# Kernel tuning notes

Measured on AMD Instinct MI355X. Metric: run time of the kernel, lower is better.

## Reference

```python
import jax, jax.numpy as jnp
from jax import lax
import numpy as np

NBC, NAC, KF, RHO = 14, 45, 52, 0.05
KT = np.arange(0.8, 0, -1.0 / 64, dtype=np.float32)[None, :]  # (1, 52) AC kernel time axis
K = KT.shape[1]


def _sigm(x, off, slope):
    return jax.nn.sigmoid(slope * (x - off))


def _ac_kernel(log_tr, log_td, kt):
    tr = jnp.exp(log_tr)[:, None]  # (nAC,1)
    td = jnp.exp(log_td)[:, None]
    k = jnp.exp(-kt / td) - jnp.exp(-(td + tr) / (td * tr) * kt)  # (nAC,K)
    return k / jnp.linalg.norm(k, axis=1, keepdims=True)


def setup_inputs() -> dict:
    key = jax.random.key(0)
    ks = jax.random.split(key, 12)
    B, T = 64, 4096
    n = 0.01  # noise_init_scale
    return {
        "x": jax.random.normal(ks[0], (B, T), jnp.float32) * 0.5,
        "bc_kernels": jax.random.normal(ks[1], (NBC, KF), jnp.float32) * 0.1,
        "log_sigmoid_slope": jnp.log(2.0) + n * jax.random.normal(ks[2], (NBC,), jnp.float32),
        "sigmoid_offset": 1.5 + n * jax.random.normal(ks[3], (NBC,), jnp.float32),
        "log_bc_ac_weight": jnp.log(1.0 / NBC) + n * jax.random.normal(ks[4], (NAC, NBC), jnp.float32),
        "log_ac_tau_rise": jnp.log(0.1) + n * jax.random.normal(ks[5], (NAC,), jnp.float32),
        "log_ac_tau_decay": jnp.log(0.1) + n * jax.random.normal(ks[6], (NAC,), jnp.float32),
        "log_ac_sigmoid_slope": jnp.log(2.0) + n * jax.random.normal(ks[7], (NAC,), jnp.float32),
        "ac_sigmoid_offset": 1.5 + n * jax.random.normal(ks[8], (NAC,), jnp.float32),
        "log_ac_bc_weight": jnp.log(0.01) + n * jax.random.normal(ks[9], (NBC, NAC), jnp.float32),
        "out_scale": jnp.ones((NBC,), jnp.float32),
    }


def reference(x, bc_kernels, log_sigmoid_slope, sigmoid_offset, log_bc_ac_weight,
              log_ac_tau_rise, log_ac_tau_decay, log_ac_sigmoid_slope,
              ac_sigmoid_offset, log_ac_bc_weight, out_scale):
    B, T = x.shape
    kt = jnp.asarray(KT)
    # linear_filter: causal conv of stimulus with per-BC kernels -> (T, B, nBC)
    xf = lax.conv_general_dilated(x[:, None, :], bc_kernels[:, None, :], (1,), [(KF - 1, 0)])
    xf = jnp.transpose(xf, (2, 0, 1))  # (T, B, nBC)

    slope = jnp.exp(log_sigmoid_slope)
    ac_slope = jnp.exp(log_ac_sigmoid_slope)
    bc_ac_w = jnp.exp(log_bc_ac_weight)          # (nAC, nBC)
    ac_bc_w = -jnp.exp(log_ac_bc_weight)         # (nBC, nAC)
    ack = _ac_kernel(log_ac_tau_rise, log_ac_tau_decay, kt)  # (nAC, K)

    # --- plain LNR branch (no feedback) ---
    prob_lnr = _sigm(xf, sigmoid_offset, slope)

    def lnr_step(pool, p):
        pool2 = pool + (1.0 - pool) * RHO
        rel = p * pool2
        return pool2 - rel, rel

    _, rel_lnr = lax.scan(lnr_step, jnp.ones((B, NBC), x.dtype), prob_lnr)
    y_lnr = (out_scale * rel_lnr).transpose(1, 0, 2)  # (B, T, nBC)

    # --- BCN branch with AC feedback recurrence ---
    def bcn_step(carry, xt):
        pool, prev_rel, buf = carry
        # append previous release (track_release[i-1]) to sliding window (oldest first)
        buf = jnp.concatenate([buf[..., 1:], prev_rel[..., None]], axis=-1)  # (B, nBC, K)
        drive = jnp.einsum('ak,ab,nbk->na', ack, bc_ac_w, buf)               # (B, nAC)
        ac_out = _sigm(drive, ac_sigmoid_offset, ac_slope)
        fb = ac_out @ ac_bc_w.T                                              # (B, nBC)
        prob = _sigm(xt + fb, sigmoid_offset, slope)
        pool2 = pool + (1.0 - pool) * RHO
        rel = prob * pool2
        return (pool2 - rel, rel, buf), (rel, fb, ac_out)

    init = (jnp.ones((B, NBC), x.dtype), jnp.zeros((B, NBC), x.dtype), jnp.zeros((B, NBC, K), x.dtype))
    _, (rel, fb, ac_out) = lax.scan(bcn_step, init, xf)
    y_bcn = (out_scale * rel).transpose(1, 0, 2)  # (B, T, nBC)
    return y_bcn, fb.transpose(1, 0, 2), ac_out.transpose(1, 0, 2), y_lnr
```

## Files before the change

kernel.cpp:

```cpp
#include <hip/hip_runtime.h>
#include <hip/hip_fp16.h>

#define NBC 14
#define NAC 45
#define KF  52
#define RHO 0.05f
#define TT  4096
#define BB  64
#define CHC 64
#define WU  44
#define NPAIR 32
#define NTW (WU + CHC)
#define SPAN (WU + 2*CHC)
#define XPAD 176
#define RING 52
#define LOG2E 1.44269504f

typedef __fp16 v2h __attribute__((ext_vector_type(2)));
typedef float  f2  __attribute__((ext_vector_type(2)));
typedef int    i2v __attribute__((ext_vector_type(2)));

__device__ __forceinline__ v2h bch(unsigned u) { return __builtin_bit_cast(v2h, u); }
__device__ __forceinline__ unsigned bcu(v2h h) { return __builtin_bit_cast(unsigned, h); }
__device__ __forceinline__ v2h pk2(float lo, float hi) {
#if __has_builtin(__builtin_amdgcn_cvt_pkrtz)
  return __builtin_bit_cast(v2h, __builtin_amdgcn_cvt_pkrtz(lo, hi));
#else
  v2h r; r[0] = (__fp16)lo; r[1] = (__fp16)hi; return r;
#endif
}
__device__ __forceinline__ v2h xsum16h(v2h v) {
#if __has_builtin(__builtin_amdgcn_permlane16_swap)
  i2v r = __builtin_amdgcn_permlane16_swap((int)bcu(v), (int)bcu(v), false, false);
  return bch((unsigned)r[0]) + bch((unsigned)r[1]);
#else
  return v + bch((unsigned)__builtin_amdgcn_ds_swizzle((int)bcu(v), (16 << 10) | 0x1f));
#endif
}
__device__ __forceinline__ v2h xsum32h(v2h v) {
#if __has_builtin(__builtin_amdgcn_permlane32_swap)
  i2v r = __builtin_amdgcn_permlane32_swap((int)bcu(v), (int)bcu(v), false, false);
  return bch((unsigned)r[0]) + bch((unsigned)r[1]);
#else
  return v + bch((unsigned)__shfl_xor((int)bcu(v), 32));
#endif
}
__device__ __forceinline__ float exp2_f(float x) {
#if __has_builtin(__builtin_amdgcn_exp2f)
  return __builtin_amdgcn_exp2f(x);
#else
  return exp2f(x);
#endif
}

#define POOL_BYTES 14608

__global__ __launch_bounds__(64)
void bcn_kernel(const float* __restrict__ x,
                const float* __restrict__ bck,
                const float* __restrict__ lss,
                const float* __restrict__ soff,
                const float* __restrict__ lbaw,
                const float* __restrict__ ltr,
                const float* __restrict__ ltd,
                const float* __restrict__ lass,
                const float* __restrict__ asoff,
                const float* __restrict__ labw,
                const float* __restrict__ oscale,
                float* __restrict__ out)
{
  __shared__ __align__(16) char pool[POOL_BYTES];
  unsigned* u_ring = (unsigned*)pool;
  float*    x_lds  = (float*)pool;
  __half*   xf_lds = (__half*)(pool + 9360);
  unsigned* acr    = (unsigned*)(pool + 14288);
  unsigned* relr   = (unsigned*)(pool + 14544);

  const int lid   = threadIdx.x;
  const int c16   = lid & 15;
  const int q     = lid >> 4;
  const int blk   = blockIdx.x;
  const int b     = blk >> 5;
  const int p     = blk & 31;
  const int t0A   = p * (2 * CHC);
  const int t_begin = t0A - WU;

  for (int i = lid; i < SPAN + KF - 1; i += 64) {
    int gt = t_begin - (KF - 1) + i;
    x_lds[i] = (gt >= 0) ? x[b * TT + gt] : 0.f;
  }
  __syncthreads();

  for (int ib = 0; ib < 3; ++ib) {
    int tau = lid + (ib << 6);
    if (tau < SPAN) {
      float acc[NBC];
#pragma unroll
      for (int c = 0; c < NBC; ++c) acc[c] = 0.f;
#pragma unroll 4
      for (int k = 0; k < KF; ++k) {
        float xv = x_lds[tau + k];
#pragma unroll
        for (int c = 0; c < NBC; ++c) acc[c] = fmaf(bck[c * KF + k], xv, acc[c]);
      }
#pragma unroll
      for (int c = 0; c < NBC; ++c) xf_lds[c * XPAD + tau] = __float2half(acc[c]);
    }
  }
  __syncthreads();

  for (int i = lid; i < NAC * RING; i += 64) u_ring[i] = 0u;
  if (lid < 64) acr[lid] = 0u;
  if (lid < 16) relr[lid] = 0u;

  float slope2 = 0.f, soff2 = 0.f, osc_c = 0.f;
  f2 poolA; poolA.x = 1.f; poolA.y = 1.f;
  f2 poolB; poolB.x = 1.f; poolB.y = 1.f;
  f2 SA; SA.x = 0.f; SA.y = 0.f;
  f2 SB; SB.x = 0.f; SB.y = 0.f;
  f2 rv2, cn2, co2; rv2.x = rv2.y = cn2.x = cn2.y = co2.x = co2.y = 0.f;
  float Adrv2 = 0.f, Boff2 = 0.f;
  v2h wfbh[16];
  v2h wuh[NBC];
  f2 yst[4], fst[4], lst[4];
  unsigned acst[4];

#pragma unroll
  for (int j = 0; j < 16; ++j) wfbh[j] = pk2(0.f, 0.f);
#pragma unroll
  for (int c = 0; c < NBC; ++c) wuh[c] = pk2(0.f, 0.f);

  if (c16 < NBC) {
    float sl = expf(lss[c16]);
    slope2 = sl * LOG2E;
    soff2  = soff[c16] * sl * LOG2E;
    osc_c  = oscale[c16];
#pragma unroll
    for (int j = 0; j < 16; ++j) {
      int a = 16 * q + j;
      if (a < NAC) { float w = -expf(labw[c16 * NAC + a]); wfbh[j] = pk2(w, w); }
    }
  }
  if (lid < NAC) {
    float tr = expf(ltr[lid]);
    float td = expf(ltd[lid]);
    float a1 = 1.f / td;
    float gg = (td + tr) / (td * tr);
    rv2.x = expf(-a1 * 0.015625f);  rv2.y = expf(-gg * 0.015625f);
    cn2.x = expf(-a1 * 0.003125f);  cn2.y = expf(-gg * 0.003125f);
    co2.x = expf(-a1 * 0.815625f);  co2.y = expf(-gg * 0.815625f);
    float nrm = 0.f;
    for (int k = 0; k < KF; ++k) {
      float kt = 0.8f - (float)k * 0.015625f;
      float d = expf(-a1 * kt) - expf(-gg * kt);
      nrm = fmaf(d, d, nrm);
    }
    float inorm  = 1.f / sqrtf(nrm);
    float aslope = expf(lass[lid]);
    Adrv2 = aslope * inorm * LOG2E;
    Boff2 = aslope * asoff[lid] * LOG2E;
#pragma unroll
    for (int c = 0; c < NBC; ++c) {
      float w = expf(lbaw[lid * NBC + c]);
      wuh[c] = pk2(w, w);
    }
  }

  float* yb  = out;
  float* fbp = out + (size_t)BB * TT * NBC;
  float* acp = out + 2 * (size_t)BB * TT * NBC;
  float* ylp = out + 2 * (size_t)BB * TT * NBC + (size_t)BB * TT * NAC;

  __syncthreads();

  auto step = [&](int slot4, int rslot, float xfA, float xfB, float uoA, float uoB,
                  bool emit) __attribute__((always_inline)) {
    float mzA = fmaf(-Adrv2, SA.x - SA.y, Boff2);
    float mzB = fmaf(-Adrv2, SB.x - SB.y, Boff2);
    float acA = __fdividef(1.f, 1.f + exp2_f(mzA));
    float acB = __fdividef(1.f, 1.f + exp2_f(mzB));
    if (lid < NAC) acr[lid] = bcu(pk2(acA, acB));

    const uint4* ab = (const uint4*)(acr + (q << 4));
    uint4 A0 = ab[0], A1 = ab[1], A2 = ab[2], A3 = ab[3];
    v2h g0 = wfbh[0] * bch(A0.x);
    v2h g1 = wfbh[1] * bch(A0.y);
    g0 += wfbh[2]  * bch(A0.z);  g1 += wfbh[3]  * bch(A0.w);
    g0 += wfbh[4]  * bch(A1.x);  g1 += wfbh[5]  * bch(A1.y);
    g0 += wfbh[6]  * bch(A1.z);  g1 += wfbh[7]  * bch(A1.w);
    g0 += wfbh[8]  * bch(A2.x);  g1 += wfbh[9]  * bch(A2.y);
    g0 += wfbh[10] * bch(A2.z);  g1 += wfbh[11] * bch(A2.w);
    g0 += wfbh[12] * bch(A3.x);  g1 += wfbh[13] * bch(A3.y);
    g0 += wfbh[14] * bch(A3.z);  g1 += wfbh[15] * bch(A3.w);
    v2h gs = xsum32h(xsum16h(g0 + g1));
    float fbA = (float)gs[0], fbB = (float)gs[1];

    float mlzA = fmaf(-slope2, xfA, soff2);
    float mpzA = fmaf(-slope2, fbA, mlzA);
    float mlzB = fmaf(-slope2, xfB, soff2);
    float mpzB = fmaf(-slope2, fbB, mlzB);
    f2 pvA, pvB;
    pvA.x = __fdividef(1.f, 1.f + exp2_f(mpzA));
    pvA.y = __fdividef(1.f, 1.f + exp2_f(mlzA));
    pvB.x = __fdividef(1.f, 1.f + exp2_f(mpzB));
    pvB.y = __fdividef(1.f, 1.f + exp2_f(mlzB));
    f2 p2A = poolA * (1.f - RHO) + RHO;
    f2 p2B = poolB * (1.f - RHO) + RHO;
    f2 rvA = pvA * p2A, rvB = pvB * p2B;
    poolA = p2A - rvA;  poolB = p2B - rvB;
    if (lid < NBC) relr[lid] = bcu(pk2(rvA.x, rvB.x));
    if (emit) {
      f2 t1; t1.x = osc_c * rvA.x; t1.y = osc_c * rvB.x; yst[slot4] = t1;
      f2 t2; t2.x = fbA;           t2.y = fbB;           fst[slot4] = t2;
      f2 t3; t3.x = osc_c * rvA.y; t3.y = osc_c * rvB.y; lst[slot4] = t3;
      acst[slot4] = bcu(pk2(acA, acB));
    }

    const uint4* rb = (const uint4*)relr;
    uint4 R0 = rb[0], R1 = rb[1], R2 = rb[2], R3 = rb[3];
    v2h h0 = wuh[0] * bch(R0.x);
    v2h h1 = wuh[1] * bch(R0.y);
    h0 += wuh[2]  * bch(R0.z);  h1 += wuh[3]  * bch(R0.w);
    h0 += wuh[4]  * bch(R1.x);  h1 += wuh[5]  * bch(R1.y);
    h0 += wuh[6]  * bch(R1.z);  h1 += wuh[7]  * bch(R1.w);
    h0 += wuh[8]  * bch(R2.x);  h1 += wuh[9]  * bch(R2.y);
    h0 += wuh[10] * bch(R2.z);  h1 += wuh[11] * bch(R2.w);
    h0 += wuh[12] * bch(R3.x);  h1 += wuh[13] * bch(R3.y);
    v2h uh = h0 + h1;
    float uA = (float)uh[0], uB = (float)uh[1];
    if (lid < NAC) {
      u_ring[lid * RING + rslot] = bcu(uh);
      SA = SA * rv2 + (cn2 * uA - co2 * uoA);
      SB = SB * rv2 + (cn2 * uB - co2 * uoB);
    }
  };

  auto group = [&](int s4, int r4, bool emit) __attribute__((always_inline)) {
    uint2 xa = *(const uint2*)&xf_lds[c16 * XPAD + s4];
    uint2 xb = *(const uint2*)&xf_lds[c16 * XPAD + s4 + CHC];
    int roff = ((lid < NAC) ? lid : 0) * RING + r4;
    uint4 ur = *(const uint4*)&u_ring[roff];
    v2h xA01 = bch(xa.x), xA23 = bch(xa.y);
    v2h xB01 = bch(xb.x), xB23 = bch(xb.y);
    v2h u0 = bch(ur.x), u1 = bch(ur.y), u2 = bch(ur.z), u3 = bch(ur.w);
    step(0, r4 + 0, (float)xA01[0], (float)xB01[0], (float)u0[0], (float)u0[1], emit);
    step(1, r4 + 1, (float)xA01[1], (float)xB01[1], (float)u1[0], (float)u1[1], emit);
    step(2, r4 + 2, (float)xA23[0], (float)xB23[0], (float)u2[0], (float)u2[1], emit);
    step(3, r4 + 3, (float)xA23[1], (float)xB23[1], (float)u3[0], (float)u3[1], emit);
  };

  int r4 = 0;
  for (int s4 = 0; s4 < WU; s4 += 4) {
    group(s4, r4, false);
    r4 += 4; if (r4 == RING) r4 = 0;
  }

  if (p == 0) {
    SA.x = 0.f; SA.y = 0.f;
    poolA.x = 1.f; poolA.y = 1.f;
    for (int i = lid; i < NAC * RING; i += 64) u_ring[i] &= 0xFFFF0000u;
  }

  for (int s4 = WU; s4 < NTW; s4 += 4) {
    group(s4, r4, true);
    r4 += 4; if (r4 == RING) r4 = 0;

    int tgA = t0A + (s4 - WU);
    size_t baseA = (size_t)b * TT + tgA;
    size_t obA = baseA * NBC + c16;
    size_t oaA = baseA * NAC + lid;
    if (lid < NBC) {
#pragma unroll
      for (int sl = 0; sl < 4; ++sl) {
        yb [obA + sl * NBC]                     = yst[sl].x;
        yb [obA + (size_t)CHC * NBC + sl * NBC] = yst[sl].y;
        fbp[obA + sl * NBC]                     = fst[sl].x;
        fbp[obA + (size_t)CHC * NBC + sl * NBC] = fst[sl].y;
        ylp[obA + sl * NBC]                     = lst[sl].x;
        ylp[obA + (size_t)CHC * NBC + sl * NBC] = lst[sl].y;
      }
    }
    if (lid < NAC) {
#pragma unroll
      for (int sl = 0; sl < 4; ++sl) {
        v2h h = bch(acst[sl]);
        acp[oaA + sl * NAC]                     = (float)h[0];
        acp[oaA + (size_t)CHC * NAC + sl * NAC] = (float)h[1];
      }
    }
  }
}

extern "C" void kernel_launch(void* const* d_in, const int* in_sizes, int n_in,
                              void* d_out, int out_size, void* d_ws, size_t ws_size,
                              hipStream_t stream) {
  (void)in_sizes; (void)n_in; (void)d_ws; (void)ws_size; (void)out_size;
  bcn_kernel<<<dim3(BB * NPAIR), dim3(64), 0, stream>>>(
      (const float*)d_in[0],
      (const float*)d_in[1],
      (const float*)d_in[2],
      (const float*)d_in[3],
      (const float*)d_in[4],
      (const float*)d_in[5],
      (const float*)d_in[6],
      (const float*)d_in[7],
      (const float*)d_in[8],
      (const float*)d_in[9],
      (const float*)d_in[10],
      (float*)d_out);
}
```

Baseline: 107.8 us.

## Split BCN and LNR sigmoid paths across lane rows; pad AC ring stride

Instead of having every lane evaluate both the feedback (BCN) and no-feedback (LNR) release sigmoids for both chunks, lanes in even 16-lane rows now compute the BCN path and lanes in odd rows compute the LNR path, selected by a row mask on the feedback term. This halves the per-step exp/reciprocal work and the per-lane pool state, and the LNR outputs are written by lanes 16..29. The AC ring buffer row stride is padded from 52 to 54 words and its quad read split into two 8-byte reads, meant to reduce LDS bank conflicts at the cost of slightly more LDS. It also changes the p==0 reset to only touch the A-half of the pool.

```diff
diff --git a/kernel.cpp b/kernel.cpp
--- a/kernel.cpp
+++ b/kernel.cpp
@@ -14,6 +14,7 @@
 #define SPAN (WU + 2*CHC)
 #define XPAD 176
 #define RING 52
+#define RINGP 54
 #define LOG2E 1.44269504f
 
 typedef __fp16 v2h __attribute__((ext_vector_type(2)));
@@ -53,7 +54,7 @@
 #endif
 }
 
-#define POOL_BYTES 14608
+#define POOL_BYTES 14976
 
 __global__ __launch_bounds__(64)
 void bcn_kernel(const float* __restrict__ x,
@@ -72,13 +73,14 @@
   __shared__ __align__(16) char pool[POOL_BYTES];
   unsigned* u_ring = (unsigned*)pool;
   float*    x_lds  = (float*)pool;
-  __half*   xf_lds = (__half*)(pool + 9360);
-  unsigned* acr    = (unsigned*)(pool + 14288);
-  unsigned* relr   = (unsigned*)(pool + 14544);
+  __half*   xf_lds = (__half*)(pool + 9720);
+  unsigned* acr    = (unsigned*)(pool + 14656);
+  unsigned* relr   = (unsigned*)(pool + 14912);
 
   const int lid   = threadIdx.x;
   const int c16   = lid & 15;
   const int q     = lid >> 4;
+  const float rowm = (q & 1) ? 0.f : 1.f;
   const int blk   = blockIdx.x;
   const int b     = blk >> 5;
   const int p     = blk & 31;
@@ -109,20 +111,19 @@
   }
   __syncthreads();
 
-  for (int i = lid; i < NAC * RING; i += 64) u_ring[i] = 0u;
+  for (int i = lid; i < NAC * RINGP; i += 64) u_ring[i] = 0u;
   if (lid < 64) acr[lid] = 0u;
   if (lid < 16) relr[lid] = 0u;
 
   float slope2 = 0.f, soff2 = 0.f, osc_c = 0.f;
-  f2 poolA; poolA.x = 1.f; poolA.y = 1.f;
-  f2 poolB; poolB.x = 1.f; poolB.y = 1.f;
+  f2 poolP; poolP.x = 1.f; poolP.y = 1.f;
   f2 SA; SA.x = 0.f; SA.y = 0.f;
   f2 SB; SB.x = 0.f; SB.y = 0.f;
   f2 rv2, cn2, co2; rv2.x = rv2.y = cn2.x = cn2.y = co2.x = co2.y = 0.f;
   float Adrv2 = 0.f, Boff2 = 0.f;
   v2h wfbh[16];
   v2h wuh[NBC];
-  f2 yst[4], fst[4], lst[4];
+  f2 yst[4], fst[4];
   unsigned acst[4];
 
 #pragma unroll
@@ -195,24 +196,18 @@
     v2h gs = xsum32h(xsum16h(g0 + g1));
     float fbA = (float)gs[0], fbB = (float)gs[1];
 
-    float mlzA = fmaf(-slope2, xfA, soff2);
-    float mpzA = fmaf(-slope2, fbA, mlzA);
-    float mlzB = fmaf(-slope2, xfB, soff2);
-    float mpzB = fmaf(-slope2, fbB, mlzB);
-    f2 pvA, pvB;
-    pvA.x = __fdividef(1.f, 1.f + exp2_f(mpzA));
-    pvA.y = __fdividef(1.f, 1.f + exp2_f(mlzA));
-    pvB.x = __fdividef(1.f, 1.f + exp2_f(mpzB));
-    pvB.y = __fdividef(1.f, 1.f + exp2_f(mlzB));
-    f2 p2A = poolA * (1.f - RHO) + RHO;
-    f2 p2B = poolB * (1.f - RHO) + RHO;
-    f2 rvA = pvA * p2A, rvB = pvB * p2B;
-    poolA = p2A - rvA;  poolB = p2B - rvB;
-    if (lid < NBC) relr[lid] = bcu(pk2(rvA.x, rvB.x));
+    float mA = fmaf(-slope2, fmaf(rowm, fbA, xfA), soff2);
+    float mB = fmaf(-slope2, fmaf(rowm, fbB, xfB), soff2);
+    f2 pv;
+    pv.x = __fdividef(1.f, 1.f + exp2_f(mA));
+    pv.y = __fdividef(1.f, 1.f + exp2_f(mB));
+    f2 p2 = poolP * (1.f - RHO) + RHO;
+    f2 relP = pv * p2;
+    poolP = p2 - relP;
+    if (lid < NBC) relr[lid] = bcu(pk2(relP.x, relP.y));
     if (emit) {
-      f2 t1; t1.x = osc_c * rvA.x; t1.y = osc_c * rvB.x; yst[slot4] = t1;
-      f2 t2; t2.x = fbA;           t2.y = fbB;           fst[slot4] = t2;
-      f2 t3; t3.x = osc_c * rvA.y; t3.y = osc_c * rvB.y; lst[slot4] = t3;
+      yst[slot4] = relP * osc_c;
+      f2 t; t.x = fbA; t.y = fbB; fst[slot4] = t;
       acst[slot4] = bcu(pk2(acA, acB));
     }
 
@@ -229,7 +224,7 @@
     v2h uh = h0 + h1;
     float uA = (float)uh[0], uB = (float)uh[1];
     if (lid < NAC) {
-      u_ring[lid * RING + rslot] = bcu(uh);
+      u_ring[lid * RINGP + rslot] = bcu(uh);
       SA = SA * rv2 + (cn2 * uA - co2 * uoA);
       SB = SB * rv2 + (cn2 * uB - co2 * uoB);
     }
@@ -238,11 +233,12 @@
   auto group = [&](int s4, int r4, bool emit) __attribute__((always_inline)) {
     uint2 xa = *(const uint2*)&xf_lds[c16 * XPAD + s4];
     uint2 xb = *(const uint2*)&xf_lds[c16 * XPAD + s4 + CHC];
-    int roff = ((lid < NAC) ? lid : 0) * RING + r4;
-    uint4 ur = *(const uint4*)&u_ring[roff];
+    int roff = ((lid < NAC) ? lid : 0) * RINGP + r4;
+    uint2 ur01 = *(const uint2*)&u_ring[roff];
+    uint2 ur23 = *(const uint2*)&u_ring[roff + 2];
     v2h xA01 = bch(xa.x), xA23 = bch(xa.y);
     v2h xB01 = bch(xb.x), xB23 = bch(xb.y);
-    v2h u0 = bch(ur.x), u1 = bch(ur.y), u2 = bch(ur.z), u3 = bch(ur.w);
+    v2h u0 = bch(ur01.x), u1 = bch(ur01.y), u2 = bch(ur23.x), u3 = bch(ur23.y);
     step(0, r4 + 0, (float)xA01[0], (float)xB01[0], (float)u0[0], (float)u0[1], emit);
     step(1, r4 + 1, (float)xA01[1], (float)xB01[1], (float)u1[0], (float)u1[1], emit);
     step(2, r4 + 2, (float)xA23[0], (float)xB23[0], (float)u2[0], (float)u2[1], emit);
@@ -257,8 +253,8 @@
 
   if (p == 0) {
     SA.x = 0.f; SA.y = 0.f;
-    poolA.x = 1.f; poolA.y = 1.f;
-    for (int i = lid; i < NAC * RING; i += 64) u_ring[i] &= 0xFFFF0000u;
+    poolP.x = 1.f;
+    for (int i = lid; i < NAC * RINGP; i += 64) u_ring[i] &= 0xFFFF0000u;
   }
 
   for (int s4 = WU; s4 < NTW; s4 += 4) {
@@ -267,25 +263,30 @@
 
     int tgA = t0A + (s4 - WU);
     size_t baseA = (size_t)b * TT + tgA;
-    size_t obA = baseA * NBC + c16;
-    size_t oaA = baseA * NAC + lid;
     if (lid < NBC) {
+      size_t ob = baseA * NBC + lid;
 #pragma unroll
       for (int sl = 0; sl < 4; ++sl) {
-        yb [obA + sl * NBC]                     = yst[sl].x;
-        yb [obA + (size_t)CHC * NBC + sl * NBC] = yst[sl].y;
-        fbp[obA + sl * NBC]                     = fst[sl].x;
-        fbp[obA + (size_t)CHC * NBC + sl * NBC] = fst[sl].y;
-        ylp[obA + sl * NBC]                     = lst[sl].x;
-        ylp[obA + (size_t)CHC * NBC + sl * NBC] = lst[sl].y;
+        yb [ob + sl * NBC]                     = yst[sl].x;
+        yb [ob + (size_t)CHC * NBC + sl * NBC] = yst[sl].y;
+        fbp[ob + sl * NBC]                     = fst[sl].x;
+        fbp[ob + (size_t)CHC * NBC + sl * NBC] = fst[sl].y;
       }
+    } else if (lid >= 16 && lid < 16 + NBC) {
+      size_t ob = baseA * NBC + (lid - 16);
+#pragma unroll
+      for (int sl = 0; sl < 4; ++sl) {
+        ylp[ob + sl * NBC]                     = yst[sl].x;
+        ylp[ob + (size_t)CHC * NBC + sl * NBC] = yst[sl].y;
+      }
     }
     if (lid < NAC) {
+      size_t oa = baseA * NAC + lid;
 #pragma unroll
       for (int sl = 0; sl < 4; ++sl) {
         v2h h = bch(acst[sl]);
-        acp[oaA + sl * NAC]                     = (float)h[0];
-        acp[oaA + (size_t)CHC * NAC + sl * NAC] = (float)h[1];
+        acp[oa + sl * NAC]                     = (float)h[0];
+        acp[oa + (size_t)CHC * NAC + sl * NAC] = (float)h[1];
       }
     }
   }
```

After: 97.41 us. 1.11x faster.
